# Optimization experiments

Measured on AMD Instinct MI355X. Metric: run time of the kernel, lower is better.

The kernel has to match this reference:

```python
import jax, jax.numpy as jnp
import numpy as np

N = 50000
E = 800000
IN = 128
HID = 128
OUT = 128
HEADS = 8
EPS = 1e-5
NEG_SLOPE = 0.2


def _gat_conv(x, src, dst, W, a_src, a_dst, b, concat):
    """PyG-style GATConv (eval mode, self-loops already appended to src/dst).
    W: [Fin, H*C], a_src/a_dst: [H, C], b: [H*C] or [C]."""
    n = x.shape[0]
    H, C = a_src.shape
    h = (x @ W).reshape(n, H, C)                      # [N,H,C]
    al_s = jnp.einsum('nhc,hc->nh', h, a_src)         # [N,H]
    al_d = jnp.einsum('nhc,hc->nh', h, a_dst)         # [N,H]
    e = jax.nn.leaky_relu(al_s[src] + al_d[dst], NEG_SLOPE)  # [E',H]
    m = jax.ops.segment_max(e, dst, num_segments=n)   # per-dst softmax (stable)
    ex = jnp.exp(e - m[dst])
    s = jax.ops.segment_sum(ex, dst, num_segments=n)
    alpha = ex / s[dst]                               # [E',H]
    out = jax.ops.segment_sum(h[src] * alpha[..., None], dst, num_segments=n)
    out = out.reshape(n, H * C) if concat else out[:, 0, :]
    return out + b


def _layernorm(x, g, b):
    mu = x.mean(-1, keepdims=True)
    var = ((x - mu) ** 2).mean(-1, keepdims=True)
    return (x - mu) * jax.lax.rsqrt(var + EPS) * g + b


def setup_inputs() -> dict:
    key = jax.random.key(0)
    ks = jax.random.split(key, 24)
    d = {}
    d['x'] = jax.random.normal(ks[0], (N, IN), jnp.float32)
    d['edge_index'] = jax.random.randint(ks[1], (2, E), 0, N)
    C = HID // HEADS
    # layer 0: in -> hidden, 8 heads, concat
    d['W0'] = jax.random.normal(ks[2], (IN, HID)) * 0.05
    d['a_src0'] = jax.random.normal(ks[3], (HEADS, C)) * 0.05
    d['a_dst0'] = jax.random.normal(ks[4], (HEADS, C)) * 0.05
    d['b0'] = jnp.zeros((HID,), jnp.float32)
    d['g0'] = jnp.ones((HID,), jnp.float32)
    d['be0'] = jnp.zeros((HID,), jnp.float32)
    # layer 1: hidden -> hidden, 8 heads, concat
    d['W1'] = jax.random.normal(ks[5], (HID, HID)) * 0.05
    d['a_src1'] = jax.random.normal(ks[6], (HEADS, C)) * 0.05
    d['a_dst1'] = jax.random.normal(ks[7], (HEADS, C)) * 0.05
    d['b1'] = jnp.zeros((HID,), jnp.float32)
    d['g1'] = jnp.ones((HID,), jnp.float32)
    d['be1'] = jnp.zeros((HID,), jnp.float32)
    # layer 2: hidden -> out, 1 head, no concat
    d['W2'] = jax.random.normal(ks[8], (HID, OUT)) * 0.05
    d['a_src2'] = jax.random.normal(ks[9], (1, OUT)) * 0.05
    d['a_dst2'] = jax.random.normal(ks[10], (1, OUT)) * 0.05
    d['b2'] = jnp.zeros((OUT,), jnp.float32)
    d['g2'] = jnp.ones((OUT,), jnp.float32)
    d['be2'] = jnp.zeros((OUT,), jnp.float32)
    return d


def reference(x, edge_index, W0, a_src0, a_dst0, b0, g0, be0,
              W1, a_src1, a_dst1, b1, g1, be1,
              W2, a_src2, a_dst2, b2, g2, be2):
    n = x.shape[0]
    loops = jnp.arange(n)
    src = jnp.concatenate([edge_index[0], loops])  # add self-loops (PyG default)
    dst = jnp.concatenate([edge_index[1], loops])

    h = _gat_conv(x, src, dst, W0, a_src0, a_dst0, b0, concat=True)
    h = jax.nn.elu(_layernorm(h, g0, be0))          # dropout: eval mode -> identity
    h = _gat_conv(h, src, dst, W1, a_src1, a_dst1, b1, concat=True)
    h = jax.nn.elu(_layernorm(h, g1, be1))
    h = _gat_conv(h, src, dst, W2, a_src2, a_dst2, b2, concat=False)
    h = _layernorm(h, g2, be2)
    return h
```

## Files before the change

### kernel.cpp

```cpp
#include <hip/hip_runtime.h>
#include <hip/hip_bf16.h>

#define NN 50000
#define EE 800000
#define EP 850000
#define DD 128
#define NB 196

#define NBUCK 196
#define BCAP 8192
#define E_PER_BLK 4096
#define GEMM_BLKS 782
#define BP1_BLKS ((EP + E_PER_BLK - 1)/E_PER_BLK)

typedef __attribute__((ext_vector_type(8))) short short8;
typedef __attribute__((ext_vector_type(4))) float f32x4;

__device__ __forceinline__ float bfu(unsigned short u){ return __uint_as_float(((unsigned)u)<<16); }
__device__ __forceinline__ unsigned short f2bs(float x){
  __hip_bfloat16 h = __float2bfloat16(x);
  union { __hip_bfloat16 h; unsigned short u; } cv; cv.h = h; return cv.u;
}

__global__ void __launch_bounds__(256) prep_kernel(
    const float* __restrict__ W0, const float* __restrict__ as0, const float* __restrict__ ad0,
    const float* __restrict__ W1, const float* __restrict__ as1, const float* __restrict__ ad1,
    const float* __restrict__ W2, const float* __restrict__ as2, const float* __restrict__ ad2,
    unsigned short* __restrict__ Wmf, int* __restrict__ bcur)
{
  const int tid = threadIdx.x;
  if (blockIdx.x == 0 && tid < NBUCK) bcur[tid] = 0;
  if (blockIdx.x < 24){
    const int L = blockIdx.x >> 3, seg = blockIdx.x & 7;
    const float* W = (L == 0) ? W0 : (L == 1) ? W1 : W2;
    int idx = seg*256 + tid;
    int t = idx >> 6, lane = idx & 63;
    int c = t >> 2, kb = t & 3;
    int m = lane & 15, quad = lane >> 4;
    unsigned short out[8];
    #pragma unroll
    for (int j = 0; j < 8; j++){
      int k = kb*32 + quad*8 + j;
      out[j] = f2bs(W[(size_t)k*DD + c*16 + m]);
    }
    *(uint4*)&Wmf[(((size_t)L*36 + t)*64 + lane)*8] = *(const uint4*)out;
  } else if (blockIdx.x < 120){
    const int q = blockIdx.x - 24;
    const int wIdx = q*4 + (tid >> 6);
    const int L = wIdx >> 7, k = wIdx & 127;
    const float *W, *as, *ad; int H;
    if (L == 0){ W = W0; as = as0; ad = ad0; H = 8; }
    else if (L == 1){ W = W1; as = as1; ad = ad1; H = 8; }
    else { W = W2; as = as2; ad = ad2; H = 1; }
    const int lane = tid & 63;
    const int c0 = lane*2;
    float w0 = W[(size_t)k*DD + c0];
    float w1 = W[(size_t)k*DD + c0 + 1];
    float ps = w0*as[c0] + w1*as[c0+1];
    float pd = w0*ad[c0] + w1*ad[c0+1];
    if (H == 8){
      #pragma unroll
      for (int off = 1; off <= 4; off <<= 1){
        ps += __shfl_xor(ps, off, 64);
        pd += __shfl_xor(pd, off, 64);
      }
    } else {
      #pragma unroll
      for (int off = 1; off <= 32; off <<= 1){
        ps += __shfl_xor(ps, off, 64);
        pd += __shfl_xor(pd, off, 64);
      }
    }
    int srcLane = (lane < 8) ? lane*8 : (lane < 16 ? (lane-8)*8 : 0);
    float vs = __shfl(ps, srcLane, 64);
    float vd = __shfl(pd, srcLane, 64);
    float myv;
    if (H == 8) myv = (lane < 8) ? vs : (lane < 16 ? vd : 0.f);
    else        myv = (lane == 0) ? ps : (lane == 1 ? pd : 0.f);
    const int kb = k >> 5, quad = (k >> 3) & 3, j = k & 7;
    if (lane < 16)
      Wmf[(((size_t)L*36 + 32 + kb)*64 + quad*16 + lane)*8 + j] = f2bs(myv);
  }
}

__device__ __forceinline__ void bp1_body(int bid, const int* __restrict__ ei,
    unsigned int* __restrict__ bins, int* __restrict__ bcur, char* smem)
{
  unsigned int* st = (unsigned int*)smem;
  int* h     = (int*)(smem + 16384);
  int* lofs  = (int*)(smem + 17168);
  int* gbase = (int*)(smem + 17952);
  int* buf   = (int*)(smem + 18736);
  const int tid = threadIdx.x;
  for (int i = tid; i < NBUCK; i += 256) h[i] = 0;
  __syncthreads();

  const int e0 = bid * E_PER_BLK;
  unsigned int pk[16];
  #pragma unroll
  for (int k = 0; k < 16; k++){
    int e = e0 + k*256 + tid;
    if (e < EP){
      int s, d;
      if (e < EE){ s = ei[e]; d = ei[EE + e]; } else { s = d = e - EE; }
      int b = d >> 8;
      pk[k] = ((unsigned)s << 16) | ((unsigned)b << 8) | (unsigned)(d & 255);
      atomicAdd(&h[b], 1);
    } else pk[k] = 0xFFFFFFFFu;
  }
  __syncthreads();

  int v = (tid < NBUCK) ? h[tid] : 0;
  buf[tid] = v;
  __syncthreads();
  for (int off = 1; off < 256; off <<= 1){
    int t = (tid >= off) ? buf[tid - off] : 0;
    __syncthreads();
    buf[tid] += t;
    __syncthreads();
  }
  if (tid < NBUCK){
    lofs[tid]  = buf[tid] - v;
    gbase[tid] = (v > 0) ? atomicAdd(&bcur[tid], v) : 0;
    h[tid] = lofs[tid];
  }
  __syncthreads();

  #pragma unroll
  for (int k = 0; k < 16; k++){
    if (pk[k] != 0xFFFFFFFFu){
      int b = (pk[k] >> 8) & 255;
      int p = atomicAdd(&h[b], 1);
      st[p] = pk[k];
    }
  }
  __syncthreads();

  const int total = buf[255];
  for (int i = tid; i < total; i += 256){
    unsigned int p = st[i];
    int b = (p >> 8) & 255;
    int idx = gbase[b] + (i - lofs[b]);
    if (idx < BCAP) bins[(size_t)b * BCAP + idx] = p;
  }
}

__global__ void __launch_bounds__(256) binpass2_kernel(const unsigned int* __restrict__ bins,
    const int* __restrict__ bcur, int* __restrict__ rowStart, unsigned short* __restrict__ srcL)
{
  __shared__ int buf[256];
  __shared__ int lcnt[256];
  __shared__ int lcur[256];
  __shared__ int ebase_s, cnt_s;
  const int b = blockIdx.x;
  const int tid = threadIdx.x;

  int v = (tid < NBUCK) ? bcur[tid] : 0;
  buf[tid] = v;
  lcnt[tid] = 0;
  __syncthreads();
  for (int off = 1; off < 256; off <<= 1){
    int t = (tid >= off) ? buf[tid - off] : 0;
    __syncthreads();
    buf[tid] += t;
    __syncthreads();
  }
  if (tid == b){ ebase_s = buf[tid] - v; cnt_s = v; }
  __syncthreads();
  const int ebase = ebase_s, cnt = cnt_s;
  const unsigned int* mybins = bins + (size_t)b * BCAP;

  for (int i = tid; i < cnt; i += 256)
    atomicAdd(&lcnt[mybins[i] & 255], 1);
  __syncthreads();

  int c = lcnt[tid];
  buf[tid] = c;
  __syncthreads();
  for (int off = 1; off < 256; off <<= 1){
    int t = (tid >= off) ? buf[tid - off] : 0;
    __syncthreads();
    buf[tid] += t;
    __syncthreads();
  }
  int excl = buf[tid] - c;
  int d = (b << 8) + tid;
  if (d <= NN) rowStart[d] = ebase + excl;
  lcur[tid] = ebase + excl;
  __syncthreads();

  for (int i = tid; i < cnt; i += 256){
    unsigned int p = mybins[i];
    int pos = atomicAdd(&lcur[p & 255], 1);
    srcL[pos] = (unsigned short)(p >> 16);
  }
}

template<bool XBF16, int H>
__device__ __forceinline__ void gemm_body(int bid, const void* __restrict__ Xv,
    const unsigned short* __restrict__ Wmf,
    unsigned short* __restrict__ Hout,
    float* __restrict__ alS, float* __restrict__ alD,
    unsigned short* wl)
{
  const int tid = threadIdx.x;
  {
    const uint4* src = (const uint4*)Wmf;
    uint4* dst = (uint4*)wl;
    #pragma unroll
    for (int i = 0; i < 9; i++)
      dst[tid + i*256] = src[tid + i*256];
  }
  const int lane = tid & 63, wv = tid >> 6;
  const int r0 = bid*64 + wv*16;
  const int m = lane & 15, quad = lane >> 4;
  const int row = r0 + m;
  const bool rowOK = row < NN;

  short8 a[4];
  if (XBF16){
    const short* Xb = (const short*)Xv;
    #pragma unroll
    for (int kb = 0; kb < 4; kb++){
      if (rowOK) a[kb] = *(const short8*)&Xb[(size_t)row*DD + kb*32 + quad*8];
      else       a[kb] = (short8){0,0,0,0,0,0,0,0};
    }
  } else {
    const float* Xf = (const float*)Xv;
    #pragma unroll
    for (int kb = 0; kb < 4; kb++){
      if (rowOK){
        float4 f0 = *(const float4*)&Xf[(size_t)row*DD + kb*32 + quad*8];
        float4 f1 = *(const float4*)&Xf[(size_t)row*DD + kb*32 + quad*8 + 4];
        union { short8 v; unsigned short u[8]; } cv;
        cv.u[0]=f2bs(f0.x); cv.u[1]=f2bs(f0.y); cv.u[2]=f2bs(f0.z); cv.u[3]=f2bs(f0.w);
        cv.u[4]=f2bs(f1.x); cv.u[5]=f2bs(f1.y); cv.u[6]=f2bs(f1.z); cv.u[7]=f2bs(f1.w);
        a[kb] = cv.v;
      } else a[kb] = (short8){0,0,0,0,0,0,0,0};
    }
  }
  __syncthreads();

  f32x4 acc[9];
  #pragma unroll
  for (int c = 0; c < 9; c++) acc[c] = (f32x4){0.f,0.f,0.f,0.f};
  #pragma unroll
  for (int c = 0; c < 9; c++){
    #pragma unroll
    for (int kb = 0; kb < 4; kb++){
      short8 b = *(const short8*)&wl[((c*4 + kb)*64 + lane)*8];
      acc[c] = __builtin_amdgcn_mfma_f32_16x16x32_bf16(a[kb], b, acc[c], 0, 0, 0);
    }
  }

  #pragma unroll
  for (int c = 0; c < 8; c++){
    #pragma unroll
    for (int r = 0; r < 4; r++){
      int rw = r0 + quad*4 + r;
      if (rw < NN) Hout[(size_t)rw*DD + c*16 + m] = f2bs(acc[c][r]);
    }
  }
  #pragma unroll
  for (int r = 0; r < 4; r++){
    int rw = r0 + quad*4 + r;
    if (rw < NN){
      float v = acc[8][r];
      if (H == 8){
        if (m < 8) alS[rw*8 + m]       = v;
        else       alD[rw*8 + (m - 8)] = v;
      } else {
        if (m == 0)      alS[rw] = v;
        else if (m == 1) alD[rw] = v;
      }
    }
  }
}

template<bool XBF16, int H>
__global__ void __launch_bounds__(256) gemm_mfma_kernel(const void* __restrict__ Xv,
    const unsigned short* __restrict__ Wmf,
    unsigned short* __restrict__ Hout,
    float* __restrict__ alS, float* __restrict__ alD)
{
  __shared__ unsigned short wl[36*64*8];
  gemm_body<XBF16, H>(blockIdx.x, Xv, Wmf, Hout, alS, alD, wl);
}

template<bool XBF16, int H>
__global__ void __launch_bounds__(256) gemm_bp1_kernel(const void* __restrict__ Xv,
    const unsigned short* __restrict__ Wmf,
    unsigned short* __restrict__ Hout,
    float* __restrict__ alS, float* __restrict__ alD,
    const int* __restrict__ ei, unsigned int* __restrict__ bins, int* __restrict__ bcur)
{
  __shared__ __align__(16) char smem[36*64*8*2];
  if (blockIdx.x < GEMM_BLKS)
    gemm_body<XBF16, H>(blockIdx.x, Xv, Wmf, Hout, alS, alD, (unsigned short*)smem);
  else
    bp1_body(blockIdx.x - GEMM_BLKS, ei, bins, bcur, smem);
}

template<int H, bool FINAL>
__global__ void __launch_bounds__(256) aggln_kernel(
    const int* __restrict__ rowStart, const unsigned short* __restrict__ srcL,
    const float* __restrict__ alS, const float* __restrict__ alD,
    const unsigned short* __restrict__ hB,
    const float* __restrict__ b, const float* __restrict__ g, const float* __restrict__ be,
    void* __restrict__ outv)
{
  const int lane = threadIdx.x & 63;
  const int d    = blockIdx.x*4 + (threadIdx.x >> 6);
  const int C    = DD / H;
  const int c0   = lane*2;
  const int hd   = c0 / C;
  const int start = __builtin_amdgcn_readfirstlane(rowStart[d]);
  const int end   = __builtin_amdgcn_readfirstlane(rowStart[d+1]);
  const float aldv = alD[d*H + hd];

  float ssum = 0.f, a0 = 0.f, a1 = 0.f;
  const unsigned int* __restrict__ sw = (const unsigned int*)srcL;

  int base = start;
  while (base < end){
    const int cnt = min(127, end - base);
    const int jw0 = base >> 1;
    unsigned int myW = (jw0 + lane < (EP >> 1)) ? sw[jw0 + lane] : 0u;

    int k = 0;
    for (; k + 8 <= cnt; k += 8){
      int ss[8];
      #pragma unroll
      for (int i = 0; i < 8; i++){
        int eidx = base + k + i;
        unsigned int wv = (unsigned int)__builtin_amdgcn_readlane((int)myW, (eidx >> 1) - jw0);
        ss[i] = (eidx & 1) ? (int)(wv >> 16) : (int)(wv & 0xFFFFu);
      }
      unsigned int hw[8]; float av[8];
      #pragma unroll
      for (int i = 0; i < 8; i++) hw[i] = *(const unsigned int*)&hB[(size_t)ss[i]*DD + c0];
      #pragma unroll
      for (int i = 0; i < 8; i++) av[i] = alS[ss[i]*H + hd];
      #pragma unroll
      for (int i = 0; i < 8; i++){
        float e_ = av[i] + aldv;
        e_ = fmaxf(e_, 0.2f*e_);
        float w_ = __expf(e_);
        ssum += w_;
        a0 = fmaf(__uint_as_float(hw[i] << 16),         w_, a0);
        a1 = fmaf(__uint_as_float(hw[i] & 0xFFFF0000u), w_, a1);
      }
    }
    for (; k < cnt; k++){
      int eidx = base + k;
      unsigned int wv = (unsigned int)__builtin_amdgcn_readlane((int)myW, (eidx >> 1) - jw0);
      int s_ = (eidx & 1) ? (int)(wv >> 16) : (int)(wv & 0xFFFFu);
      unsigned int hw_ = *(const unsigned int*)&hB[(size_t)s_*DD + c0];
      float av_ = alS[s_*H + hd];
      float e_ = av_ + aldv;
      e_ = fmaxf(e_, 0.2f*e_);
      float w_ = __expf(e_);
      ssum += w_;
      a0 = fmaf(__uint_as_float(hw_ << 16),         w_, a0);
      a1 = fmaf(__uint_as_float(hw_ & 0xFFFF0000u), w_, a1);
    }
    base += cnt;
  }

  const float sinv = 1.f / ssum;

  float v0 = a0*sinv + b[c0], v1 = a1*sinv + b[c0+1];
  float s2 = v0 + v1;
  #pragma unroll
  for (int off = 32; off >= 1; off >>= 1) s2 += __shfl_xor(s2, off, 64);
  float mu = s2 * (1.0f/128.0f);
  float d0 = v0 - mu, d1 = v1 - mu;
  float q = d0*d0 + d1*d1;
  #pragma unroll
  for (int off = 32; off >= 1; off >>= 1) q += __shfl_xor(q, off, 64);
  float r = rsqrtf(q*(1.0f/128.0f) + 1e-5f);
  float y0 = d0*r*g[c0]   + be[c0];
  float y1 = d1*r*g[c0+1] + be[c0+1];
  if (FINAL){
    *(float2*)&((float*)outv)[(size_t)d*DD + c0] = make_float2(y0, y1);
  } else {
    y0 = y0 > 0.f ? y0 : __expf(y0) - 1.f;
    y1 = y1 > 0.f ? y1 : __expf(y1) - 1.f;
    ushort2 o; o.x = f2bs(y0); o.y = f2bs(y1);
    *(ushort2*)&((unsigned short*)outv)[(size_t)d*DD + c0] = o;
  }
}

extern "C" void kernel_launch(void* const* d_in, const int* in_sizes, int n_in,
                              void* d_out, int out_size, void* d_ws, size_t ws_size,
                              hipStream_t stream)
{
  char* w = (char*)d_ws;
  unsigned short* accB = (unsigned short*)w;     w += (size_t)NN*DD*2;
  unsigned short* hB   = (unsigned short*)w;     w += (size_t)NN*DD*2;
  float* alS      = (float*)w;                   w += (size_t)NN*8*4;
  float* alD      = (float*)w;                   w += (size_t)NN*8*4;
  unsigned short* Wmf = (unsigned short*)w;      w += (size_t)3*36*64*8*2;
  int*   rowStart = (int*)w;                     w += (size_t)(NN+1)*4;
  int*   bcur     = (int*)w;                     w += 1024;
  unsigned short* srcL = (unsigned short*)w;     w += (size_t)EP*2;
  if (ws_size < (size_t)(w - (char*)d_ws)) return;

  unsigned int* bins = (unsigned int*)accB;

  const float* x  = (const float*)d_in[0];
  const int*   ei = (const int*)d_in[1];
  const float *W0=(const float*)d_in[2], *as0=(const float*)d_in[3], *ad0=(const float*)d_in[4];
  const float *b0=(const float*)d_in[5], *g0=(const float*)d_in[6], *be0=(const float*)d_in[7];
  const float *W1=(const float*)d_in[8], *as1=(const float*)d_in[9], *ad1=(const float*)d_in[10];
  const float *b1=(const float*)d_in[11],*g1=(const float*)d_in[12],*be1=(const float*)d_in[13];
  const float *W2=(const float*)d_in[14],*as2=(const float*)d_in[15],*ad2=(const float*)d_in[16];
  const float *b2=(const float*)d_in[17],*g2=(const float*)d_in[18],*be2=(const float*)d_in[19];

  prep_kernel<<<NB, 256, 0, stream>>>(W0, as0, ad0, W1, as1, ad1, W2, as2, ad2, Wmf, bcur);

  gemm_bp1_kernel<false, 8><<<GEMM_BLKS + BP1_BLKS, 256, 0, stream>>>(
      x, Wmf, hB, alS, alD, ei, bins, bcur);
  binpass2_kernel<<<NBUCK, 256, 0, stream>>>(bins, bcur, rowStart, srcL);

  aggln_kernel<8, false><<<12500, 256, 0, stream>>>(rowStart, srcL, alS, alD, hB,
                                                    b0, g0, be0, accB);
  gemm_mfma_kernel<true, 8><<<GEMM_BLKS, 256, 0, stream>>>(accB, Wmf + (size_t)36*64*8,
                                                           hB, alS, alD);
  aggln_kernel<8, false><<<12500, 256, 0, stream>>>(rowStart, srcL, alS, alD, hB,
                                                    b1, g1, be1, accB);
  gemm_mfma_kernel<true, 1><<<GEMM_BLKS, 256, 0, stream>>>(accB, Wmf + (size_t)2*36*64*8,
                                                           hB, alS, alD);
  aggln_kernel<1, true><<<12500, 256, 0, stream>>>(rowStart, srcL, alS, alD, hB,
                                                   b2, g2, be2, d_out);
}
```

Before: 284.7 us.

## Precompute edge attention weights per chunk in LDS and process two edges per wave

```diff
diff --git a/kernel.cpp b/kernel.cpp
--- a/kernel.cpp
+++ b/kernel.cpp
@@ -309,85 +309,129 @@
     const float* __restrict__ b, const float* __restrict__ g, const float* __restrict__ be,
     void* __restrict__ outv)
 {
-  const int lane = threadIdx.x & 63;
-  const int d    = blockIdx.x*4 + (threadIdx.x >> 6);
-  const int C    = DD / H;
-  const int c0   = lane*2;
-  const int hd   = c0 / C;
+  __shared__ float wbuf[4][64*H];
+  const int tid  = threadIdx.x;
+  const int lane = tid & 63, wv = tid >> 6;
+  const int d    = blockIdx.x*4 + wv;
+  float* wb = wbuf[wv];
+  const int l2   = lane & 31;
+  const int half = lane >> 5;
+  const int ch0  = l2*4;
+  const int hd   = (H == 8) ? (ch0 >> 4) : 0;
+
   const int start = __builtin_amdgcn_readfirstlane(rowStart[d]);
   const int end   = __builtin_amdgcn_readfirstlane(rowStart[d+1]);
-  const float aldv = alD[d*H + hd];
-
-  float ssum = 0.f, a0 = 0.f, a1 = 0.f;
-  const unsigned int* __restrict__ sw = (const unsigned int*)srcL;
-
-  int base = start;
-  while (base < end){
-    const int cnt = min(127, end - base);
-    const int jw0 = base >> 1;
-    unsigned int myW = (jw0 + lane < (EP >> 1)) ? sw[jw0 + lane] : 0u;
-
-    int k = 0;
-    for (; k + 8 <= cnt; k += 8){
-      int ss[8];
+
+  float aldv[H];
+  #pragma unroll
+  for (int h = 0; h < H; h++) aldv[h] = alD[d*H + h];
+
+  float ssum = 0.f, a0 = 0.f, a1 = 0.f, a2 = 0.f, a3 = 0.f;
+
+  for (int base = start; base < end; base += 64){
+    const int cnt = min(64, end - base);
+    const bool act = lane < cnt;
+    int myS = 0;
+    if (act) myS = (int)srcL[base + lane];
+
+    asm volatile("s_waitcnt lgkmcnt(0)" ::: "memory");
+
+    if (H == 8){
+      float4 s0 = *(const float4*)&alS[myS*8];
+      float4 s1 = *(const float4*)&alS[myS*8 + 4];
+      float in_[8] = {s0.x, s0.y, s0.z, s0.w, s1.x, s1.y, s1.z, s1.w};
+      float wv_[8];
       #pragma unroll
-      for (int i = 0; i < 8; i++){
-        int eidx = base + k + i;
-        unsigned int wv = (unsigned int)__builtin_amdgcn_readlane((int)myW, (eidx >> 1) - jw0);
-        ss[i] = (eidx & 1) ? (int)(wv >> 16) : (int)(wv & 0xFFFFu);
-      }
-      unsigned int hw[8]; float av[8];
+      for (int h = 0; h < 8; h++){
+        float e_ = in_[h] + aldv[h];
+        e_ = fmaxf(e_, 0.2f*e_);
+        wv_[h] = act ? __expf(e_) : 0.f;
+      }
+      float4 o0 = {wv_[0], wv_[1], wv_[2], wv_[3]};
+      float4 o1 = {wv_[4], wv_[5], wv_[6], wv_[7]};
+      *(float4*)&wb[lane*8]     = o0;
+      *(float4*)&wb[lane*8 + 4] = o1;
+    } else {
+      float e_ = alS[myS] + aldv[0];
+      e_ = fmaxf(e_, 0.2f*e_);
+      wb[lane] = act ? __expf(e_) : 0.f;
+    }
+    asm volatile("s_waitcnt lgkmcnt(0)" ::: "memory");
+    __builtin_amdgcn_sched_barrier(0);
+
+    const int npair = (cnt + 1) >> 1;
+    int p = 0;
+    for (; p + 8 <= npair; p += 8){
+      uint2 hw[8]; float wt[8];
       #pragma unroll
-      for (int i = 0; i < 8; i++) hw[i] = *(const unsigned int*)&hB[(size_t)ss[i]*DD + c0];
+      for (int j = 0; j < 8; j++){
+        int e2 = 2*(p + j);
+        int sl = __builtin_amdgcn_readlane(myS, e2);
+        int sh = __builtin_amdgcn_readlane(myS, e2 + 1);
+        int se = half ? sh : sl;
+        hw[j] = *(const uint2*)&hB[(size_t)se*DD + ch0];
+        wt[j] = wb[(e2 + half)*H + hd];
+      }
       #pragma unroll
-      for (int i = 0; i < 8; i++) av[i] = alS[ss[i]*H + hd];
-      #pragma unroll
-      for (int i = 0; i < 8; i++){
-        float e_ = av[i] + aldv;
-        e_ = fmaxf(e_, 0.2f*e_);
-        float w_ = __expf(e_);
+      for (int j = 0; j < 8; j++){
+        float w_ = wt[j];
         ssum += w_;
-        a0 = fmaf(__uint_as_float(hw[i] << 16),         w_, a0);
-        a1 = fmaf(__uint_as_float(hw[i] & 0xFFFF0000u), w_, a1);
-      }
-    }
-    for (; k < cnt; k++){
-      int eidx = base + k;
-      unsigned int wv = (unsigned int)__builtin_amdgcn_readlane((int)myW, (eidx >> 1) - jw0);
-      int s_ = (eidx & 1) ? (int)(wv >> 16) : (int)(wv & 0xFFFFu);
-      unsigned int hw_ = *(const unsigned int*)&hB[(size_t)s_*DD + c0];
-      float av_ = alS[s_*H + hd];
-      float e_ = av_ + aldv;
-      e_ = fmaxf(e_, 0.2f*e_);
-      float w_ = __expf(e_);
+        a0 = fmaf(__uint_as_float(hw[j].x << 16),         w_, a0);
+        a1 = fmaf(__uint_as_float(hw[j].x & 0xFFFF0000u), w_, a1);
+        a2 = fmaf(__uint_as_float(hw[j].y << 16),         w_, a2);
+        a3 = fmaf(__uint_as_float(hw[j].y & 0xFFFF0000u), w_, a3);
+      }
+    }
+    for (; p < npair; ++p){
+      int e2 = 2*p;
+      int sl = __builtin_amdgcn_readlane(myS, e2);
+      int sh = __builtin_amdgcn_readlane(myS, e2 + 1);
+      int se = half ? sh : sl;
+      uint2 hw = *(const uint2*)&hB[(size_t)se*DD + ch0];
+      float w_ = wb[(e2 + half)*H + hd];
       ssum += w_;
-      a0 = fmaf(__uint_as_float(hw_ << 16),         w_, a0);
-      a1 = fmaf(__uint_as_float(hw_ & 0xFFFF0000u), w_, a1);
-    }
-    base += cnt;
-  }
+      a0 = fmaf(__uint_as_float(hw.x << 16),         w_, a0);
+      a1 = fmaf(__uint_as_float(hw.x & 0xFFFF0000u), w_, a1);
+      a2 = fmaf(__uint_as_float(hw.y << 16),         w_, a2);
+      a3 = fmaf(__uint_as_float(hw.y & 0xFFFF0000u), w_, a3);
+    }
+  }
+
+  ssum += __shfl_xor(ssum, 32, 64);
+  a0 += __shfl_xor(a0, 32, 64);
+  a1 += __shfl_xor(a1, 32, 64);
+  a2 += __shfl_xor(a2, 32, 64);
+  a3 += __shfl_xor(a3, 32, 64);
 
   const float sinv = 1.f / ssum;
-
-  float v0 = a0*sinv + b[c0], v1 = a1*sinv + b[c0+1];
-  float s2 = v0 + v1;
-  #pragma unroll
-  for (int off = 32; off >= 1; off >>= 1) s2 += __shfl_xor(s2, off, 64);
+  float4 bb = *(const float4*)&b[ch0];
+  float v0 = a0*sinv + bb.x, v1 = a1*sinv + bb.y;
+  float v2 = a2*sinv + bb.z, v3 = a3*sinv + bb.w;
+  float s2 = (v0 + v1) + (v2 + v3);
+  #pragma unroll
+  for (int off = 16; off >= 1; off >>= 1) s2 += __shfl_xor(s2, off, 64);
   float mu = s2 * (1.0f/128.0f);
-  float d0 = v0 - mu, d1 = v1 - mu;
-  float q = d0*d0 + d1*d1;
-  #pragma unroll
-  for (int off = 32; off >= 1; off >>= 1) q += __shfl_xor(q, off, 64);
+  float d0 = v0 - mu, d1 = v1 - mu, d2 = v2 - mu, d3 = v3 - mu;
+  float q = (d0*d0 + d1*d1) + (d2*d2 + d3*d3);
+  #pragma unroll
+  for (int off = 16; off >= 1; off >>= 1) q += __shfl_xor(q, off, 64);
   float r = rsqrtf(q*(1.0f/128.0f) + 1e-5f);
-  float y0 = d0*r*g[c0]   + be[c0];
-  float y1 = d1*r*g[c0+1] + be[c0+1];
+  float4 gg = *(const float4*)&g[ch0];
+  float4 ee = *(const float4*)&be[ch0];
+  float y0 = d0*r*gg.x + ee.x, y1 = d1*r*gg.y + ee.y;
+  float y2 = d2*r*gg.z + ee.z, y3 = d3*r*gg.w + ee.w;
   if (FINAL){
-    *(float2*)&((float*)outv)[(size_t)d*DD + c0] = make_float2(y0, y1);
+    if (half == 0)
+      *(float4*)&((float*)outv)[(size_t)d*DD + ch0] = make_float4(y0, y1, y2, y3);
   } else {
     y0 = y0 > 0.f ? y0 : __expf(y0) - 1.f;
     y1 = y1 > 0.f ? y1 : __expf(y1) - 1.f;
-    ushort2 o; o.x = f2bs(y0); o.y = f2bs(y1);
-    *(ushort2*)&((unsigned short*)outv)[(size_t)d*DD + c0] = o;
+    y2 = y2 > 0.f ? y2 : __expf(y2) - 1.f;
+    y3 = y3 > 0.f ? y3 : __expf(y3) - 1.f;
+    if (half == 0){
+      ushort4 o; o.x = f2bs(y0); o.y = f2bs(y1); o.z = f2bs(y2); o.w = f2bs(y3);
+      *(ushort4*)&((unsigned short*)outv)[(size_t)d*DD + ch0] = o;
+    }
   }
 }
 
```

Measured after the change: 295.5 us. 3.8% more time.

## Slice hidden features per head for cache-local gathers, split aggregation from layernorm

Applied to the files above, without the earlier changes.

```diff
diff --git a/kernel.cpp b/kernel.cpp
--- a/kernel.cpp
+++ b/kernel.cpp
@@ -201,7 +201,7 @@
     const unsigned short* __restrict__ Wmf,
     unsigned short* __restrict__ Hout,
     float* __restrict__ alS, float* __restrict__ alD,
-    unsigned short* wl)
+    unsigned short* wl, float (*altile)[16][17])
 {
   const int tid = threadIdx.x;
   {
@@ -258,20 +258,25 @@
     #pragma unroll
     for (int r = 0; r < 4; r++){
       int rw = r0 + quad*4 + r;
-      if (rw < NN) Hout[(size_t)rw*DD + c*16 + m] = f2bs(acc[c][r]);
-    }
-  }
-  #pragma unroll
-  for (int r = 0; r < 4; r++){
-    int rw = r0 + quad*4 + r;
+      if (rw < NN) Hout[((size_t)c*NN + rw)*16 + m] = f2bs(acc[c][r]);
+    }
+  }
+  #pragma unroll
+  for (int r = 0; r < 4; r++) altile[wv][m][quad*4 + r] = acc[8][r];
+  asm volatile("s_waitcnt lgkmcnt(0)" ::: "memory");
+  __builtin_amdgcn_sched_barrier(0);
+  #pragma unroll
+  for (int p = 0; p < 4; p++){
+    int h16 = p*4 + quad;
+    int rw = r0 + m;
+    float v = altile[wv][h16][m];
     if (rw < NN){
-      float v = acc[8][r];
       if (H == 8){
-        if (m < 8) alS[rw*8 + m]       = v;
-        else       alD[rw*8 + (m - 8)] = v;
+        if (h16 < 8) alS[(size_t)h16*NN + rw] = v;
+        else         alD[(size_t)(h16-8)*NN + rw] = v;
       } else {
-        if (m == 0)      alS[rw] = v;
-        else if (m == 1) alD[rw] = v;
+        if (h16 == 0)      alS[rw] = v;
+        else if (h16 == 1) alD[rw] = v;
       }
     }
   }
@@ -284,7 +289,8 @@
     float* __restrict__ alS, float* __restrict__ alD)
 {
   __shared__ unsigned short wl[36*64*8];
-  gemm_body<XBF16, H>(blockIdx.x, Xv, Wmf, Hout, alS, alD, wl);
+  __shared__ float altile[4][16][17];
+  gemm_body<XBF16, H>(blockIdx.x, Xv, Wmf, Hout, alS, alD, wl, altile);
 }
 
 template<bool XBF16, int H>
@@ -295,81 +301,72 @@
     const int* __restrict__ ei, unsigned int* __restrict__ bins, int* __restrict__ bcur)
 {
   __shared__ __align__(16) char smem[36*64*8*2];
+  __shared__ float altile[4][16][17];
   if (blockIdx.x < GEMM_BLKS)
-    gemm_body<XBF16, H>(blockIdx.x, Xv, Wmf, Hout, alS, alD, (unsigned short*)smem);
+    gemm_body<XBF16, H>(blockIdx.x, Xv, Wmf, Hout, alS, alD, (unsigned short*)smem, altile);
   else
     bp1_body(blockIdx.x - GEMM_BLKS, ei, bins, bcur, smem);
 }
 
-template<int H, bool FINAL>
-__global__ void __launch_bounds__(256) aggln_kernel(
+template<int H>
+__global__ void __launch_bounds__(256) sliceagg_kernel(
     const int* __restrict__ rowStart, const unsigned short* __restrict__ srcL,
-    const float* __restrict__ alS, const float* __restrict__ alD,
+    const float* __restrict__ alS_t, const float* __restrict__ alD_t,
     const unsigned short* __restrict__ hB,
+    float* __restrict__ temp)
+{
+  const int tid  = threadIdx.x;
+  const int lane = tid & 63, wv = tid >> 6;
+  const int blk  = blockIdx.x;
+  const int s    = blk & 7;
+  const int d    = (blk >> 3)*4 + wv;
+  const int eg   = lane >> 4, ch = lane & 15;
+  const int hoff = (H == 8) ? s : 0;
+
+  const unsigned short* __restrict__ hS = hB + (size_t)s*NN*16;
+  const float* __restrict__ aS = alS_t + (size_t)hoff*NN;
+
+  const int start = __builtin_amdgcn_readfirstlane(rowStart[d]);
+  const int end   = __builtin_amdgcn_readfirstlane(rowStart[d+1]);
+  const float aldv = alD_t[(size_t)hoff*NN + d];
+
+  float ssum = 0.f, acc = 0.f;
+  for (int base = start; base < end; base += 8){
+    int e0 = base + eg, e1 = base + 4 + eg;
+    bool v0 = e0 < end, v1 = e1 < end;
+    int s0 = v0 ? (int)srcL[e0] : 0;
+    int s1 = v1 ? (int)srcL[e1] : 0;
+    unsigned short h0 = hS[(size_t)s0*16 + ch];
+    unsigned short h1 = hS[(size_t)s1*16 + ch];
+    float al0 = aS[s0], al1 = aS[s1];
+    float x0 = al0 + aldv; x0 = fmaxf(x0, 0.2f*x0);
+    float x1 = al1 + aldv; x1 = fmaxf(x1, 0.2f*x1);
+    float w0 = v0 ? __expf(x0) : 0.f;
+    float w1 = v1 ? __expf(x1) : 0.f;
+    ssum += w0 + w1;
+    acc = fmaf(bfu(h0), w0, acc);
+    acc = fmaf(bfu(h1), w1, acc);
+  }
+  ssum += __shfl_xor(ssum, 16, 64);
+  ssum += __shfl_xor(ssum, 32, 64);
+  acc  += __shfl_xor(acc, 16, 64);
+  acc  += __shfl_xor(acc, 32, 64);
+  if (lane < 16)
+    temp[(size_t)d*DD + s*16 + ch] = acc / ssum;
+}
+
+template<bool FINAL>
+__global__ void __launch_bounds__(256) aggfin_kernel(
+    const float* __restrict__ temp,
     const float* __restrict__ b, const float* __restrict__ g, const float* __restrict__ be,
     void* __restrict__ outv)
 {
   const int lane = threadIdx.x & 63;
   const int d    = blockIdx.x*4 + (threadIdx.x >> 6);
-  const int C    = DD / H;
   const int c0   = lane*2;
-  const int hd   = c0 / C;
-  const int start = __builtin_amdgcn_readfirstlane(rowStart[d]);
-  const int end   = __builtin_amdgcn_readfirstlane(rowStart[d+1]);
-  const float aldv = alD[d*H + hd];
-
-  float ssum = 0.f, a0 = 0.f, a1 = 0.f;
-  const unsigned int* __restrict__ sw = (const unsigned int*)srcL;
-
-  int base = start;
-  while (base < end){
-    const int cnt = min(127, end - base);
-    const int jw0 = base >> 1;
-    unsigned int myW = (jw0 + lane < (EP >> 1)) ? sw[jw0 + lane] : 0u;
-
-    int k = 0;
-    for (; k + 8 <= cnt; k += 8){
-      int ss[8];
-      #pragma unroll
-      for (int i = 0; i < 8; i++){
-        int eidx = base + k + i;
-        unsigned int wv = (unsigned int)__builtin_amdgcn_readlane((int)myW, (eidx >> 1) - jw0);
-        ss[i] = (eidx & 1) ? (int)(wv >> 16) : (int)(wv & 0xFFFFu);
-      }
-      unsigned int hw[8]; float av[8];
-      #pragma unroll
-      for (int i = 0; i < 8; i++) hw[i] = *(const unsigned int*)&hB[(size_t)ss[i]*DD + c0];
-      #pragma unroll
-      for (int i = 0; i < 8; i++) av[i] = alS[ss[i]*H + hd];
-      #pragma unroll
-      for (int i = 0; i < 8; i++){
-        float e_ = av[i] + aldv;
-        e_ = fmaxf(e_, 0.2f*e_);
-        float w_ = __expf(e_);
-        ssum += w_;
-        a0 = fmaf(__uint_as_float(hw[i] << 16),         w_, a0);
-        a1 = fmaf(__uint_as_float(hw[i] & 0xFFFF0000u), w_, a1);
-      }
-    }
-    for (; k < cnt; k++){
-      int eidx = base + k;
-      unsigned int wv = (unsigned int)__builtin_amdgcn_readlane((int)myW, (eidx >> 1) - jw0);
-      int s_ = (eidx & 1) ? (int)(wv >> 16) : (int)(wv & 0xFFFFu);
-      unsigned int hw_ = *(const unsigned int*)&hB[(size_t)s_*DD + c0];
-      float av_ = alS[s_*H + hd];
-      float e_ = av_ + aldv;
-      e_ = fmaxf(e_, 0.2f*e_);
-      float w_ = __expf(e_);
-      ssum += w_;
-      a0 = fmaf(__uint_as_float(hw_ << 16),         w_, a0);
-      a1 = fmaf(__uint_as_float(hw_ & 0xFFFF0000u), w_, a1);
-    }
-    base += cnt;
-  }
-
-  const float sinv = 1.f / ssum;
-
-  float v0 = a0*sinv + b[c0], v1 = a1*sinv + b[c0+1];
+
+  float2 t = *(const float2*)&temp[(size_t)d*DD + c0];
+  float v0 = t.x + b[c0], v1 = t.y + b[c0+1];
   float s2 = v0 + v1;
   #pragma unroll
   for (int off = 32; off >= 1; off >>= 1) s2 += __shfl_xor(s2, off, 64);
@@ -400,6 +397,7 @@
   unsigned short* hB   = (unsigned short*)w;     w += (size_t)NN*DD*2;
   float* alS      = (float*)w;                   w += (size_t)NN*8*4;
   float* alD      = (float*)w;                   w += (size_t)NN*8*4;
+  float* temp     = (float*)w;                   w += (size_t)NN*DD*4;
   unsigned short* Wmf = (unsigned short*)w;      w += (size_t)3*36*64*8*2;
   int*   rowStart = (int*)w;                     w += (size_t)(NN+1)*4;
   int*   bcur     = (int*)w;                     w += 1024;
@@ -423,14 +421,16 @@
       x, Wmf, hB, alS, alD, ei, bins, bcur);
   binpass2_kernel<<<NBUCK, 256, 0, stream>>>(bins, bcur, rowStart, srcL);
 
-  aggln_kernel<8, false><<<12500, 256, 0, stream>>>(rowStart, srcL, alS, alD, hB,
-                                                    b0, g0, be0, accB);
+  sliceagg_kernel<8><<<12500*8, 256, 0, stream>>>(rowStart, srcL, alS, alD, hB, temp);
+  aggfin_kernel<false><<<12500, 256, 0, stream>>>(temp, b0, g0, be0, accB);
+
   gemm_mfma_kernel<true, 8><<<GEMM_BLKS, 256, 0, stream>>>(accB, Wmf + (size_t)36*64*8,
                                                            hB, alS, alD);
-  aggln_kernel<8, false><<<12500, 256, 0, stream>>>(rowStart, srcL, alS, alD, hB,
-                                                    b1, g1, be1, accB);
+  sliceagg_kernel<8><<<12500*8, 256, 0, stream>>>(rowStart, srcL, alS, alD, hB, temp);
+  aggfin_kernel<false><<<12500, 256, 0, stream>>>(temp, b1, g1, be1, accB);
+
   gemm_mfma_kernel<true, 1><<<GEMM_BLKS, 256, 0, stream>>>(accB, Wmf + (size_t)2*36*64*8,
                                                            hB, alS, alD);
-  aggln_kernel<1, true><<<12500, 256, 0, stream>>>(rowStart, srcL, alS, alD, hB,
-                                                   b2, g2, be2, d_out);
-}
+  sliceagg_kernel<1><<<12500*8, 256, 0, stream>>>(rowStart, srcL, alS, alD, hB, temp);
+  aggfin_kernel<true><<<12500, 256, 0, stream>>>(temp, b2, g2, be2, d_out);
+}
```

After: 597.2 us. 110% more time.

## Stage GEMM output through LDS for coalesced stores; simplify edge-index loop

Applied to the files above, without the earlier changes.

```diff
diff --git a/kernel.cpp b/kernel.cpp
--- a/kernel.cpp
+++ b/kernel.cpp
@@ -254,14 +254,6 @@
   }
 
   #pragma unroll
-  for (int c = 0; c < 8; c++){
-    #pragma unroll
-    for (int r = 0; r < 4; r++){
-      int rw = r0 + quad*4 + r;
-      if (rw < NN) Hout[(size_t)rw*DD + c*16 + m] = f2bs(acc[c][r]);
-    }
-  }
-  #pragma unroll
   for (int r = 0; r < 4; r++){
     int rw = r0 + quad*4 + r;
     if (rw < NN){
@@ -275,6 +267,28 @@
       }
     }
   }
+
+  __syncthreads();
+  unsigned short* ht = wl;
+  const int lr = wv*16 + quad*4;
+  #pragma unroll
+  for (int c = 0; c < 8; c++){
+    #pragma unroll
+    for (int r = 0; r < 4; r++)
+      ht[(lr + r)*136 + c*16 + m] = f2bs(acc[c][r]);
+  }
+  __syncthreads();
+  const int r0b = bid*64;
+  #pragma unroll
+  for (int p = 0; p < 4; p++){
+    int i = p*256 + tid;
+    int lrow = i >> 4, chunk = i & 15;
+    int grow = r0b + lrow;
+    if (grow < NN){
+      uint4 v = *(const uint4*)((const char*)ht + lrow*272 + chunk*16);
+      *(uint4*)&Hout[(size_t)grow*DD + chunk*8] = v;
+    }
+  }
 }
 
 template<bool XBF16, int H>
@@ -321,51 +335,37 @@
   float ssum = 0.f, a0 = 0.f, a1 = 0.f;
   const unsigned int* __restrict__ sw = (const unsigned int*)srcL;
 
-  int base = start;
-  while (base < end){
-    const int cnt = min(127, end - base);
-    const int jw0 = base >> 1;
-    unsigned int myW = (jw0 + lane < (EP >> 1)) ? sw[jw0 + lane] : 0u;
-
-    int k = 0;
-    for (; k + 8 <= cnt; k += 8){
-      int ss[8];
-      #pragma unroll
-      for (int i = 0; i < 8; i++){
-        int eidx = base + k + i;
-        unsigned int wv = (unsigned int)__builtin_amdgcn_readlane((int)myW, (eidx >> 1) - jw0);
-        ss[i] = (eidx & 1) ? (int)(wv >> 16) : (int)(wv & 0xFFFFu);
-      }
-      unsigned int hw[8]; float av[8];
-      #pragma unroll
-      for (int i = 0; i < 8; i++) hw[i] = *(const unsigned int*)&hB[(size_t)ss[i]*DD + c0];
-      #pragma unroll
-      for (int i = 0; i < 8; i++) av[i] = alS[ss[i]*H + hd];
-      #pragma unroll
-      for (int i = 0; i < 8; i++){
-        float e_ = av[i] + aldv;
-        e_ = fmaxf(e_, 0.2f*e_);
-        float w_ = __expf(e_);
-        ssum += w_;
-        a0 = fmaf(__uint_as_float(hw[i] << 16),         w_, a0);
-        a1 = fmaf(__uint_as_float(hw[i] & 0xFFFF0000u), w_, a1);
-      }
-    }
-    for (; k < cnt; k++){
-      int eidx = base + k;
-      unsigned int wv = (unsigned int)__builtin_amdgcn_readlane((int)myW, (eidx >> 1) - jw0);
-      int s_ = (eidx & 1) ? (int)(wv >> 16) : (int)(wv & 0xFFFFu);
-      unsigned int hw_ = *(const unsigned int*)&hB[(size_t)s_*DD + c0];
-      float av_ = alS[s_*H + hd];
-      float e_ = av_ + aldv;
-      e_ = fmaxf(e_, 0.2f*e_);
-      float w_ = __expf(e_);
-      ssum += w_;
-      a0 = fmaf(__uint_as_float(hw_ << 16),         w_, a0);
-      a1 = fmaf(__uint_as_float(hw_ & 0xFFFF0000u), w_, a1);
-    }
-    base += cnt;
-  }
+  #define PROC(sv) { \
+    int s_ = (sv); \
+    const unsigned short* hr_ = hB + (size_t)s_*DD; \
+    const float* ar_ = alS + s_*H; \
+    unsigned int hw_ = *(const unsigned int*)&hr_[c0]; \
+    float e_ = ar_[hd] + aldv; \
+    e_ = fmaxf(e_, 0.2f*e_); \
+    float w_ = __expf(e_); \
+    ssum += w_; \
+    a0 = fmaf(__uint_as_float(hw_ << 16),          w_, a0); \
+    a1 = fmaf(__uint_as_float(hw_ & 0xFFFF0000u),  w_, a1); \
+  }
+
+  int jw = start >> 1;
+  if (start & 1){
+    unsigned int w = sw[jw]; PROC((int)(w >> 16)); jw++;
+  }
+  const int jwF = end >> 1;
+  for (; jw + 2 <= jwF; jw += 2){
+    unsigned int w0 = sw[jw], w1 = sw[jw+1];
+    PROC((int)(w0 & 0xFFFFu)); PROC((int)(w0 >> 16));
+    PROC((int)(w1 & 0xFFFFu)); PROC((int)(w1 >> 16));
+  }
+  for (; jw < jwF; ++jw){
+    unsigned int w = sw[jw];
+    PROC((int)(w & 0xFFFFu)); PROC((int)(w >> 16));
+  }
+  if (end & 1){
+    unsigned int w = sw[jwF]; PROC((int)(w & 0xFFFFu));
+  }
+  #undef PROC
 
   const float sinv = 1.f / ssum;
 
```

Result: faster. 275.6 us (-3.2%).
